# Performance work log

Measured on AMD Instinct MI355X. Metric: run time of the kernel, lower is better.

Reference implementation:

```python
import jax, jax.numpy as jnp
import numpy as np

OUT_F, IN_F = 8192, 4096
TOKENS = 512


def _unpack_int2_to_ternary(packed, alpha, dtype):
    # packed: [out_f, in_f//4] ints 0..255; 4 two-bit codes per byte.
    # code 0 -> -1, code 2 -> +1, codes 1/3 -> 0; then scale by per-row alpha.
    shifts = jnp.arange(4, dtype=packed.dtype) * 2  # [0,2,4,6]
    two_bit = (packed[:, :, None] >> shifts[None, None, :]) & 3  # [out_f, in_f//4, 4]
    two_bit = two_bit.reshape(packed.shape[0], -1)  # [out_f, in_f]
    sign = jnp.where(two_bit == 2, 1.0, jnp.where(two_bit == 0, -1.0, 0.0)).astype(dtype)
    return sign * alpha.astype(dtype)[:, None]


def setup_inputs() -> dict:
    key = jax.random.key(0)
    k1, k2, k3, k4 = jax.random.split(key, 4)
    x = jax.random.normal(k1, (TOKENS, IN_F), dtype=jnp.float32)
    weight_int2 = jax.random.randint(k2, (OUT_F, IN_F // 4), 0, 256, dtype=jnp.int32)
    alpha = jax.random.uniform(k3, (OUT_F,), dtype=jnp.float32, minval=0.01, maxval=0.05)
    bias = jax.random.normal(k4, (OUT_F,), dtype=jnp.float32) * 0.01
    return {"x": x, "weight_int2": weight_int2, "alpha": alpha, "bias": bias}


def reference(x, weight_int2, alpha, bias):
    W = _unpack_int2_to_ternary(weight_int2, alpha, x.dtype)  # [out_f, in_f]
    out = x @ W.T  # [tokens, out_f]
    return out + bias
```

## Files before the change

### kernel.cpp

```cpp
#include <hip/hip_runtime.h>
#include <hip/hip_bf16.h>

typedef unsigned int u32;
typedef unsigned short u16;

#define TOKENS 512
#define OUT_F  8192
#define IN_F   4096
#define KPACK  (IN_F / 4)
#define TMB 128
#define TNB 128
#define BKW 128
#define NWIN (IN_F / BKW)

typedef __attribute__((ext_vector_type(8))) short bf16x8;
typedef __attribute__((ext_vector_type(4))) float f32x4;
typedef __attribute__((ext_vector_type(16))) float f32x16;

__device__ __forceinline__ u32 pack_bf16x2(float a, float b) {
    __hip_bfloat162 h = __float22bfloat162_rn(make_float2(a, b));
    union { __hip_bfloat162 h2; u32 u; } cvt;
    cvt.h2 = h;
    return cvt.u;
}

__device__ __forceinline__ u32 decode_pair(u32 d) {
    u32 s = (__umul24(d, 0x808202u) & 0x06060606u) + 0x01000100u;
    return __builtin_amdgcn_perm(0x00003F80u, 0x0000BF80u, s);
}
__device__ __forceinline__ bf16x8 decode_frag(u32 w, int sh) {
    union { bf16x8 v; u32 u[4]; } c;
    c.u[0] = decode_pair((w >> (sh + 0)) & 0xFu);
    c.u[1] = decode_pair((w >> (sh + 4)) & 0xFu);
    c.u[2] = decode_pair((w >> (sh + 8)) & 0xFu);
    c.u[3] = decode_pair((w >> (sh + 12)) & 0xFu);
    return c.v;
}

__device__ __forceinline__ void async_ld16(const void* g, void* l) {
    __builtin_amdgcn_global_load_lds(
        (const __attribute__((address_space(1))) u32*)g,
        (__attribute__((address_space(3))) u32*)l, 16, 0, 0);
}

__device__ __forceinline__ void async_b(const uint2* g, uint2& dst) {
    asm volatile("global_load_dwordx2 %0, %1, off"
                 : "=v"(dst) : "v"(g) : "memory");
}

#define VMW(N) asm volatile("s_waitcnt vmcnt(" #N ")" ::: "memory")

__global__ __launch_bounds__(256) void prep(const float* __restrict__ X,
                                            u16* __restrict__ Xb,
                                            const u32* __restrict__ W2,
                                            uint2* __restrict__ W7) {
    __shared__ u32 dense[128 * 32];
    const int t = threadIdx.x;

    if (blockIdx.y == 8) {
        int base = blockIdx.x * 32768 + t * 8;
#pragma unroll
        for (int r = 0; r < 16; ++r) {
            int i = base + r * 2048;
            float4 a = *(const float4*)(X + i);
            float4 b = *(const float4*)(X + i + 4);
            uint4 q;
            q.x = pack_bf16x2(a.x, a.y);
            q.y = pack_bf16x2(a.z, a.w);
            q.z = pack_bf16x2(b.x, b.y);
            q.w = pack_bf16x2(b.z, b.w);
            *(uint4*)(Xb + i) = q;
        }
        return;
    }

    const int ngrp = blockIdx.x;
    const int kc   = blockIdx.y;
#pragma unroll
    for (int i = 0; i < 16; ++i) {
        int id = t + 256 * i;
        int col = id >> 5, jq = id & 31;
        uint4 wv = *(const uint4*)(W2 + (size_t)(ngrp * 128 + col) * KPACK + kc * 128 + jq * 4);
        dense[col * 32 + (jq ^ (col & 31))] =
            (wv.x & 0xFFu) | ((wv.y & 0xFFu) << 8) | ((wv.z & 0xFFu) << 16) | ((wv.w & 0xFFu) << 24);
    }
    __syncthreads();
    const u16* sp = (const u16*)dense;
#pragma unroll
    for (int p = 0; p < 8; ++p) {
        int e = t + 256 * p;
        int lane = e & 63;
        int kq = (e >> 6) & 3;
        int wloc = (e >> 8) & 3;
        int nh = (e >> 10) & 1;
        int h = lane >> 5;
        int c0 = nh * 64 + (lane & 31), c1 = c0 + 32;
        int j0 = wloc * 8 + kq * 2;
        u32 x0 = sp[((c0 * 32 + (j0 ^ (c0 & 31))) << 1) | h];
        u32 x1 = sp[((c0 * 32 + ((j0 + 1) ^ (c0 & 31))) << 1) | h];
        u32 y0 = sp[((c1 * 32 + (j0 ^ (c1 & 31))) << 1) | h];
        u32 y1 = sp[((c1 * 32 + ((j0 + 1) ^ (c1 & 31))) << 1) | h];
        uint2 o;
        o.x = x0 | (x1 << 16);
        o.y = y0 | (y1 << 16);
        int w = kc * 4 + wloc;
        W7[(((size_t)(ngrp * 2 + nh) * 32 + w) * 4 + kq) * 64 + lane] = o;
    }
}

__global__ __launch_bounds__(512, 2) void ternary_gemm11(
    const u16* __restrict__ Xb,
    const uint2* __restrict__ W7,
    const float* __restrict__ alpha,
    const float* __restrict__ bias,
    float* __restrict__ Out)
{
    __shared__ u16 As[4][TMB * BKW];

    const int tid  = threadIdx.x;
    const int lane = tid & 63;
    const int wave = tid >> 6;
    const int kq = wave & 3;
    const int nh = wave >> 2;

    const int m0 = blockIdx.x * TMB;
    const int ngrp = blockIdx.y;
    const int n0 = ngrp * TNB;

    f32x16 acc[4][2];
#pragma unroll
    for (int mt = 0; mt < 4; ++mt)
#pragma unroll
        for (int nt = 0; nt < 2; ++nt)
#pragma unroll
            for (int i = 0; i < 16; ++i)
                acc[mt][nt][i] = 0.f;

    const u16* ga[4];
    u32 lbase[4];
#pragma unroll
    for (int i = 0; i < 4; ++i) {
        int rbase = wave * 16 + i * 4;
        int row = rbase + (lane >> 4);
        int cd = (lane & 15) ^ (row & 15);
        ga[i] = Xb + (size_t)(m0 + row) * IN_F + cd * 8;
        lbase[i] = rbase * BKW;
    }

    int ofsA[4][2];
#pragma unroll
    for (int mt = 0; mt < 4; ++mt)
#pragma unroll
        for (int ks = 0; ks < 2; ++ks) {
            int row = mt * 32 + (lane & 31);
            int chunk = kq * 4 + ks * 2 + (lane >> 5);
            ofsA[mt][ks] = row * BKW + ((chunk ^ (row & 15))) * 8;
        }

    const uint2* wp = W7 + ((size_t)(ngrp * 2 + nh) * NWIN * 4 + kq) * 64 + lane;

    auto issueA = [&](int w) {
        u16* d = As[w & 3];
        const int koff = w * BKW;
#pragma unroll
        for (int i = 0; i < 4; ++i)
            async_ld16(ga[i] + koff, d + lbase[i]);
    };

    auto window_compute = [&](int buf, uint2 bq) {
        const u16* ab = As[buf];
#pragma unroll
        for (int ks = 0; ks < 2; ++ks) {
            bf16x8 a0 = *(const bf16x8*)(ab + ofsA[0][ks]);
            bf16x8 a1 = *(const bf16x8*)(ab + ofsA[1][ks]);
            bf16x8 a2 = *(const bf16x8*)(ab + ofsA[2][ks]);
            bf16x8 a3 = *(const bf16x8*)(ab + ofsA[3][ks]);
            bf16x8 b0 = decode_frag(bq.x, ks * 16);
            bf16x8 b1 = decode_frag(bq.y, ks * 16);
            acc[0][0] = __builtin_amdgcn_mfma_f32_32x32x16_bf16(a0, b0, acc[0][0], 0, 0, 0);
            acc[1][0] = __builtin_amdgcn_mfma_f32_32x32x16_bf16(a1, b0, acc[1][0], 0, 0, 0);
            acc[2][0] = __builtin_amdgcn_mfma_f32_32x32x16_bf16(a2, b0, acc[2][0], 0, 0, 0);
            acc[3][0] = __builtin_amdgcn_mfma_f32_32x32x16_bf16(a3, b0, acc[3][0], 0, 0, 0);
            acc[0][1] = __builtin_amdgcn_mfma_f32_32x32x16_bf16(a0, b1, acc[0][1], 0, 0, 0);
            acc[1][1] = __builtin_amdgcn_mfma_f32_32x32x16_bf16(a1, b1, acc[1][1], 0, 0, 0);
            acc[2][1] = __builtin_amdgcn_mfma_f32_32x32x16_bf16(a2, b1, acc[2][1], 0, 0, 0);
            acc[3][1] = __builtin_amdgcn_mfma_f32_32x32x16_bf16(a3, b1, acc[3][1], 0, 0, 0);
        }
    };

    uint2 bqE, bqO;
    async_b(wp, bqE);
    issueA(0);
    async_b(wp + 256, bqO);
    issueA(1);

#pragma unroll 1
    for (int p = 0; p < (NWIN - 2) / 2; ++p) {
        const int w = 2 * p;
        VMW(5);
        __builtin_amdgcn_s_barrier();
        __builtin_amdgcn_sched_barrier(0);
        window_compute(w & 3, bqE);
        async_b(wp + (size_t)(w + 2) * 256, bqE);
        issueA(w + 2);

        VMW(5);
        __builtin_amdgcn_s_barrier();
        __builtin_amdgcn_sched_barrier(0);
        window_compute((w + 1) & 3, bqO);
        async_b(wp + (size_t)(w + 3) * 256, bqO);
        issueA(w + 3);
    }
    VMW(5);
    __builtin_amdgcn_s_barrier();
    __builtin_amdgcn_sched_barrier(0);
    window_compute(30 & 3, bqE);
    VMW(0);
    __builtin_amdgcn_s_barrier();
    __builtin_amdgcn_sched_barrier(0);
    window_compute(31 & 3, bqO);

    f32x4* red = (f32x4*)As;
#pragma unroll 1
    for (int q = 1; q < 4; ++q) {
        if (kq == q) {
            f32x4* dst = red + nh * 2048 + lane;
#pragma unroll
            for (int mt = 0; mt < 4; ++mt)
#pragma unroll
                for (int nt = 0; nt < 2; ++nt)
#pragma unroll
                    for (int sub = 0; sub < 4; ++sub) {
                        f32x4 v = {acc[mt][nt][sub * 4 + 0], acc[mt][nt][sub * 4 + 1],
                                   acc[mt][nt][sub * 4 + 2], acc[mt][nt][sub * 4 + 3]};
                        dst[(mt * 8 + nt * 4 + sub) * 64] = v;
                    }
        }
        __syncthreads();
        if (kq == 0) {
            const f32x4* src = red + nh * 2048 + lane;
#pragma unroll
            for (int mt = 0; mt < 4; ++mt)
#pragma unroll
                for (int nt = 0; nt < 2; ++nt)
#pragma unroll
                    for (int sub = 0; sub < 4; ++sub) {
                        f32x4 v = src[(mt * 8 + nt * 4 + sub) * 64];
#pragma unroll
                        for (int i = 0; i < 4; ++i)
                            acc[mt][nt][sub * 4 + i] += v[i];
                    }
        }
        __syncthreads();
    }

    if (kq == 0) {
#pragma unroll
        for (int nt = 0; nt < 2; ++nt) {
            int ncol = n0 + nh * 64 + nt * 32 + (lane & 31);
            float av = alpha[ncol];
            float bv = bias[ncol];
#pragma unroll
            for (int mt = 0; mt < 4; ++mt) {
#pragma unroll
                for (int r = 0; r < 16; ++r) {
                    int row = m0 + mt * 32 + (r & 3) + 8 * (r >> 2) + 4 * (lane >> 5);
                    Out[(size_t)row * OUT_F + ncol] = acc[mt][nt][r] * av + bv;
                }
            }
        }
    }
}

__global__ void ternary_naive(const float* __restrict__ X, const u32* __restrict__ W2,
                              const float* __restrict__ alpha, const float* __restrict__ bias,
                              float* __restrict__ Out) {
    int o  = blockIdx.x * 64 + (threadIdx.x & 63);
    int tk = blockIdx.y * 4 + (threadIdx.x >> 6);
    const float* x = X + (size_t)tk * IN_F;
    const u32* w = W2 + (size_t)o * KPACK;
    float s = 0.f;
    for (int d = 0; d < KPACK; ++d) {
        u32 b = w[d] & 0xFFu;
        const float* xp = x + d * 4;
#pragma unroll
        for (int j = 0; j < 4; ++j) {
            u32 c = (b >> (2 * j)) & 3u;
            float wv = (c == 2u) ? 1.f : ((c == 0u) ? -1.f : 0.f);
            s += xp[j] * wv;
        }
    }
    Out[(size_t)tk * OUT_F + o] = s * alpha[o] + bias[o];
}

extern "C" void kernel_launch(void* const* d_in, const int* in_sizes, int n_in,
                              void* d_out, int out_size, void* d_ws, size_t ws_size,
                              hipStream_t stream) {
    const float* x = (const float*)d_in[0];
    const u32* w2 = (const u32*)d_in[1];
    const float* alpha = (const float*)d_in[2];
    const float* bias  = (const float*)d_in[3];
    float* out = (float*)d_out;

    const size_t xb_bytes = (size_t)TOKENS * IN_F * sizeof(u16);
    const size_t w7_bytes = (size_t)OUT_F * IN_F / 4;

    if (ws_size >= xb_bytes + w7_bytes) {
        u16* xb = (u16*)d_ws;
        uint2* w7 = (uint2*)((char*)d_ws + xb_bytes);
        prep<<<dim3(64, 9), 256, 0, stream>>>(x, xb, w2, w7);
        ternary_gemm11<<<dim3(TOKENS / TMB, OUT_F / TNB), 512, 0, stream>>>(xb, w7, alpha, bias, out);
    } else {
        ternary_naive<<<dim3(OUT_F / 64, TOKENS / 4), 256, 0, stream>>>(x, w2, alpha, bias, out);
    }
}
```

Baseline: 126.9 us.

## Double K-window width with 2-stage A buffering and dwordx4 weight fragments

Doubles the K window to 256 columns, switching the A shared-memory ring from 4 buffers of 128 to 2 buffers of 256. The pipeline now issues the next window's A load just before computing the current one. The prep kernel repacks weights so each lane fetches a 16-byte fragment per window with dwordx4, halving the number of barriers and B load instructions. In exchange the prefetch depth drops from two windows ahead to one, which may expose memory latency. The A load and read swizzle is also changed to fit the wider rows.

Result: no change. 126.5 us (-0.3%).

```diff
diff --git a/kernel.cpp b/kernel.cpp
--- a/kernel.cpp
+++ b/kernel.cpp
@@ -10,7 +10,7 @@
 #define KPACK  (IN_F / 4)
 #define TMB 128
 #define TNB 128
-#define BKW 128
+#define BKW 256
 #define NWIN (IN_F / BKW)
 
 typedef __attribute__((ext_vector_type(8))) short bf16x8;
@@ -43,8 +43,8 @@
         (__attribute__((address_space(3))) u32*)l, 16, 0, 0);
 }
 
-__device__ __forceinline__ void async_b(const uint2* g, uint2& dst) {
-    asm volatile("global_load_dwordx2 %0, %1, off"
+__device__ __forceinline__ void async_b4(const uint4* g, uint4& dst) {
+    asm volatile("global_load_dwordx4 %0, %1, off"
                  : "=v"(dst) : "v"(g) : "memory");
 }
 
@@ -53,7 +53,7 @@
 __global__ __launch_bounds__(256) void prep(const float* __restrict__ X,
                                             u16* __restrict__ Xb,
                                             const u32* __restrict__ W2,
-                                            uint2* __restrict__ W7) {
+                                            uint4* __restrict__ W10) {
     __shared__ u32 dense[128 * 32];
     const int t = threadIdx.x;
 
@@ -87,35 +87,39 @@
     __syncthreads();
     const u16* sp = (const u16*)dense;
 #pragma unroll
-    for (int p = 0; p < 8; ++p) {
+    for (int p = 0; p < 4; ++p) {
         int e = t + 256 * p;
         int lane = e & 63;
         int kq = (e >> 6) & 3;
-        int wloc = (e >> 8) & 3;
-        int nh = (e >> 10) & 1;
+        int nh = (e >> 8) & 1;
+        int wloc = (e >> 9) & 1;
         int h = lane >> 5;
         int c0 = nh * 64 + (lane & 31), c1 = c0 + 32;
-        int j0 = wloc * 8 + kq * 2;
-        u32 x0 = sp[((c0 * 32 + (j0 ^ (c0 & 31))) << 1) | h];
-        u32 x1 = sp[((c0 * 32 + ((j0 + 1) ^ (c0 & 31))) << 1) | h];
-        u32 y0 = sp[((c1 * 32 + (j0 ^ (c1 & 31))) << 1) | h];
-        u32 y1 = sp[((c1 * 32 + ((j0 + 1) ^ (c1 & 31))) << 1) | h];
-        uint2 o;
-        o.x = x0 | (x1 << 16);
-        o.y = y0 | (y1 << 16);
-        int w = kc * 4 + wloc;
-        W7[(((size_t)(ngrp * 2 + nh) * 32 + w) * 4 + kq) * 64 + lane] = o;
-    }
-}
-
-__global__ __launch_bounds__(512, 2) void ternary_gemm11(
+        u32 f[4], g[4];
+#pragma unroll
+        for (int ks = 0; ks < 4; ++ks) {
+            int j = wloc * 16 + kq * 4 + ks;
+            f[ks] = sp[((c0 * 32 + (j ^ (c0 & 31))) << 1) | h];
+            g[ks] = sp[((c1 * 32 + (j ^ (c1 & 31))) << 1) | h];
+        }
+        uint4 o;
+        o.x = f[0] | (f[1] << 16);
+        o.y = f[2] | (f[3] << 16);
+        o.z = g[0] | (g[1] << 16);
+        o.w = g[2] | (g[3] << 16);
+        int w = kc * 2 + wloc;
+        W10[(((size_t)(ngrp * 2 + nh) * 4 + kq) * NWIN + w) * 64 + lane] = o;
+    }
+}
+
+__global__ __launch_bounds__(512, 2) void ternary_gemm14(
     const u16* __restrict__ Xb,
-    const uint2* __restrict__ W7,
+    const uint4* __restrict__ W10,
     const float* __restrict__ alpha,
     const float* __restrict__ bias,
     float* __restrict__ Out)
 {
-    __shared__ u16 As[4][TMB * BKW];
+    __shared__ u16 As[2][TMB * BKW];
 
     const int tid  = threadIdx.x;
     const int lane = tid & 63;
@@ -136,47 +140,50 @@
             for (int i = 0; i < 16; ++i)
                 acc[mt][nt][i] = 0.f;
 
-    const u16* ga[4];
-    u32 lbase[4];
-#pragma unroll
-    for (int i = 0; i < 4; ++i) {
-        int rbase = wave * 16 + i * 4;
-        int row = rbase + (lane >> 4);
-        int cd = (lane & 15) ^ (row & 15);
-        ga[i] = Xb + (size_t)(m0 + row) * IN_F + cd * 8;
-        lbase[i] = rbase * BKW;
-    }
-
-    int ofsA[4][2];
-#pragma unroll
-    for (int mt = 0; mt < 4; ++mt)
-#pragma unroll
-        for (int ks = 0; ks < 2; ++ks) {
-            int row = mt * 32 + (lane & 31);
-            int chunk = kq * 4 + ks * 2 + (lane >> 5);
-            ofsA[mt][ks] = row * BKW + ((chunk ^ (row & 15))) * 8;
-        }
-
-    const uint2* wp = W7 + ((size_t)(ngrp * 2 + nh) * NWIN * 4 + kq) * 64 + lane;
+    const u16* gbase = Xb + (size_t)(m0 + wave * 16) * IN_F;
+    u32 aoff[8];
+    u32 lbase[8];
+#pragma unroll
+    for (int i = 0; i < 8; ++i) {
+        int rr = i * 2 + (lane >> 5);
+        int cd = ((lane & 15) ^ (rr & 15)) | (lane & 16);
+        aoff[i] = rr * IN_F + cd * 8;
+        lbase[i] = (wave * 16 + i * 2) * BKW;
+    }
+
+    u32 ofsA0[4];
+#pragma unroll
+    for (int ks = 0; ks < 4; ++ks) {
+        int row = lane & 31;
+        int chunk = kq * 8 + ks * 2 + (lane >> 5);
+        int slot = ((chunk & 15) ^ (row & 15)) | (chunk & 16);
+        ofsA0[ks] = row * BKW + slot * 8;
+    }
+
+    const uint4* wq = W10 + (((size_t)(ngrp * 2 + nh) * 4 + kq) * NWIN) * 64 + lane;
 
     auto issueA = [&](int w) {
-        u16* d = As[w & 3];
+        u16* d = As[w & 1];
         const int koff = w * BKW;
 #pragma unroll
-        for (int i = 0; i < 4; ++i)
-            async_ld16(ga[i] + koff, d + lbase[i]);
+        for (int i = 0; i < 8; ++i)
+            async_ld16(gbase + aoff[i] + koff, d + lbase[i]);
     };
 
-    auto window_compute = [&](int buf, uint2 bq) {
+    auto window_compute = [&](int buf, uint4 bq) {
         const u16* ab = As[buf];
 #pragma unroll
-        for (int ks = 0; ks < 2; ++ks) {
-            bf16x8 a0 = *(const bf16x8*)(ab + ofsA[0][ks]);
-            bf16x8 a1 = *(const bf16x8*)(ab + ofsA[1][ks]);
-            bf16x8 a2 = *(const bf16x8*)(ab + ofsA[2][ks]);
-            bf16x8 a3 = *(const bf16x8*)(ab + ofsA[3][ks]);
-            bf16x8 b0 = decode_frag(bq.x, ks * 16);
-            bf16x8 b1 = decode_frag(bq.y, ks * 16);
+        for (int ks = 0; ks < 4; ++ks) {
+            const u16* ap = ab + ofsA0[ks];
+            bf16x8 a0 = *(const bf16x8*)(ap);
+            bf16x8 a1 = *(const bf16x8*)(ap + 8192);
+            bf16x8 a2 = *(const bf16x8*)(ap + 16384);
+            bf16x8 a3 = *(const bf16x8*)(ap + 24576);
+            u32 wx = (ks < 2) ? bq.x : bq.y;
+            u32 wz = (ks < 2) ? bq.z : bq.w;
+            const int sh = (ks & 1) * 16;
+            bf16x8 b0 = decode_frag(wx, sh);
+            bf16x8 b1 = decode_frag(wz, sh);
             acc[0][0] = __builtin_amdgcn_mfma_f32_32x32x16_bf16(a0, b0, acc[0][0], 0, 0, 0);
             acc[1][0] = __builtin_amdgcn_mfma_f32_32x32x16_bf16(a1, b0, acc[1][0], 0, 0, 0);
             acc[2][0] = __builtin_amdgcn_mfma_f32_32x32x16_bf16(a2, b0, acc[2][0], 0, 0, 0);
@@ -188,37 +195,37 @@
         }
     };
 
-    uint2 bqE, bqO;
-    async_b(wp, bqE);
+    uint4 bqE, bqO;
+    async_b4(wq, bqE);
     issueA(0);
-    async_b(wp + 256, bqO);
-    issueA(1);
+    async_b4(wq + 64, bqO);
 
 #pragma unroll 1
     for (int p = 0; p < (NWIN - 2) / 2; ++p) {
         const int w = 2 * p;
-        VMW(5);
+        VMW(1);
         __builtin_amdgcn_s_barrier();
         __builtin_amdgcn_sched_barrier(0);
-        window_compute(w & 3, bqE);
-        async_b(wp + (size_t)(w + 2) * 256, bqE);
-        issueA(w + 2);
-
-        VMW(5);
+        issueA(w + 1);
+        window_compute(0, bqE);
+        async_b4(wq + (size_t)(w + 2) * 64, bqE);
+
+        VMW(1);
         __builtin_amdgcn_s_barrier();
         __builtin_amdgcn_sched_barrier(0);
-        window_compute((w + 1) & 3, bqO);
-        async_b(wp + (size_t)(w + 3) * 256, bqO);
-        issueA(w + 3);
-    }
-    VMW(5);
+        issueA(w + 2);
+        window_compute(1, bqO);
+        async_b4(wq + (size_t)(w + 3) * 64, bqO);
+    }
+    VMW(1);
     __builtin_amdgcn_s_barrier();
     __builtin_amdgcn_sched_barrier(0);
-    window_compute(30 & 3, bqE);
+    issueA(15);
+    window_compute(0, bqE);
     VMW(0);
     __builtin_amdgcn_s_barrier();
     __builtin_amdgcn_sched_barrier(0);
-    window_compute(31 & 3, bqO);
+    window_compute(1, bqO);
 
     f32x4* red = (f32x4*)As;
 #pragma unroll 1
@@ -302,14 +309,14 @@
     const float* bias  = (const float*)d_in[3];
     float* out = (float*)d_out;
 
-    const size_t xb_bytes = (size_t)TOKENS * IN_F * sizeof(u16);
-    const size_t w7_bytes = (size_t)OUT_F * IN_F / 4;
-
-    if (ws_size >= xb_bytes + w7_bytes) {
+    const size_t xb_bytes  = (size_t)TOKENS * IN_F * sizeof(u16);
+    const size_t w10_bytes = (size_t)OUT_F * IN_F / 4;
+
+    if (ws_size >= xb_bytes + w10_bytes) {
         u16* xb = (u16*)d_ws;
-        uint2* w7 = (uint2*)((char*)d_ws + xb_bytes);
-        prep<<<dim3(64, 9), 256, 0, stream>>>(x, xb, w2, w7);
-        ternary_gemm11<<<dim3(TOKENS / TMB, OUT_F / TNB), 512, 0, stream>>>(xb, w7, alpha, bias, out);
+        uint4* w10 = (uint4*)((char*)d_ws + xb_bytes);
+        prep<<<dim3(64, 9), 256, 0, stream>>>(x, xb, w2, w10);
+        ternary_gemm14<<<dim3(TOKENS / TMB, OUT_F / TNB), 512, 0, stream>>>(xb, w10, alpha, bias, out);
     } else {
         ternary_naive<<<dim3(OUT_F / 64, TOKENS / 4), 256, 0, stream>>>(x, w2, alpha, bias, out);
     }
```
